# Performance work log

Hardware: AMD Instinct MI355X
Metric: run time of the kernel (lower is better)

The kernel has to match this reference:

```python
import jax, jax.numpy as jnp
import numpy as np
import math

TEMPERATURE = 1.0
TOP_K = 8
STALENESS_LAMBDA = 0.005
STALENESS_FLOOR = 0.1

B, F, H, E = 2048, 512, 256, 64


def setup_inputs() -> dict:
    key = jax.random.key(0)
    ks = jax.random.split(key, 9)
    return {
        "features": jax.random.normal(ks[0], (B, F), jnp.float32),
        "proj_w": jax.random.normal(ks[1], (H, F), jnp.float32) * (1.0 / math.sqrt(F)),
        "proj_b": jnp.zeros((H,), jnp.float32),
        "expert_emb": jax.random.normal(ks[2], (E, H), jnp.float32) * 0.1,  # nn.init.normal_(std=0.1)
        "expert_features": jax.random.normal(ks[3], (E, F), jnp.float32),
        "trust": jax.random.uniform(ks[4], (E,), jnp.float32, 0.1, 1.0),
        "staleness_dt": jax.random.uniform(ks[5], (E,), jnp.float32, 0.0, 600.0),  # seconds since update
        "fst_w": jax.random.normal(ks[6], (E, F, F), jnp.float32) * (1.0 / math.sqrt(F)),
        "fst_b": jnp.zeros((E, F), jnp.float32),
    }


def reference(features, proj_w, proj_b, expert_emb, expert_features, trust,
              staleness_dt, fst_w, fst_b):
    # --- learned gating: sigmoid(proj(x) . emb_j / sqrt(hidden_dim)) ---
    h = features @ proj_w.T + proj_b                      # [B,H]
    gate_logits = (h @ expert_emb.T) / jnp.sqrt(jnp.float32(h.shape[-1]))  # [B,E]
    gate = jax.nn.sigmoid(gate_logits)

    # --- similarity S_ij: cosine, clamped at 0 ---
    fn = features / jnp.maximum(jnp.linalg.norm(features, axis=1, keepdims=True), 1e-8)
    en = expert_features / jnp.maximum(jnp.linalg.norm(expert_features, axis=1, keepdims=True), 1e-8)
    sim = jnp.clip(fn @ en.T, 0.0, None)                  # [B,E]

    # --- staleness factor: max(floor, exp(-lambda * dt)) ---
    stale = jnp.maximum(STALENESS_FLOOR, jnp.exp(-STALENESS_LAMBDA * staleness_dt))  # [E]

    # --- final score: gate * T * S * staleness ---
    score = gate * sim * (trust * stale)[None, :]          # [B,E]

    # --- top-k expert selection + temperature softmax over selected ---
    top_v, top_i = jax.lax.top_k(score, TOP_K)             # [B,K]
    w = jax.nn.softmax(top_v / TEMPERATURE, axis=-1)       # [B,K]

    # --- per-expert FST (linear feature-space transform), MoE aggregation ---
    y = jnp.einsum('bf,efg->beg', features, fst_w) + fst_b[None]   # [B,E,F]
    yk = jnp.take_along_axis(y, top_i[:, :, None], axis=1)          # [B,K,F]
    out = jnp.einsum('bk,bkf->bf', w, yk)                           # [B,F]
    return out
```

## Files before the change

kernel.cpp:

```cpp
#include <hip/hip_runtime.h>
#include <hip/hip_fp16.h>
#include <math.h>

#define B_N 2048
#define F_N 512
#define H_N 256
#define E_N 64

typedef __attribute__((ext_vector_type(8))) _Float16 half8;
typedef __attribute__((ext_vector_type(4))) float f32x4;


__global__ __launch_bounds__(256) void k_prep(
    const float* __restrict__ proj_w, const float* __restrict__ expert_emb,
    const float* __restrict__ expert_features, const float* __restrict__ trust,
    const float* __restrict__ dt, const float* __restrict__ features,
    const float* __restrict__ fst_w, float* __restrict__ pwT,
    float* __restrict__ embT, float* __restrict__ enT,
    float* __restrict__ coef, int* __restrict__ cnt, _Float16* __restrict__ Fh,
    _Float16* __restrict__ Fl, float* __restrict__ fnorm,
    _Float16* __restrict__ WhT) {
  __shared__ float tile[16704];
  __shared__ float parts[4];
  int bid = blockIdx.x, tid = threadIdx.x;
  if (bid < 512) {
    int idx = bid * 256 + tid;
    int f = idx >> 8, h = idx & 255;
    pwT[idx] = proj_w[h * 512 + f];
    if (bid == 0 && tid < E_N) cnt[tid] = 0;
  } else if (bid < 576) {
    int e = bid - 512;
    float v0 = expert_features[e * 512 + tid];
    float v1 = expert_features[e * 512 + tid + 256];
    float ss = v0 * v0 + v1 * v1;
    #pragma unroll
    for (int off = 32; off; off >>= 1) ss += __shfl_xor(ss, off);
    if ((tid & 63) == 0) parts[tid >> 6] = ss;
    __syncthreads();
    float tot = parts[0] + parts[1] + parts[2] + parts[3];
    float inv = 1.0f / fmaxf(sqrtf(tot), 1e-8f);
    enT[tid * 64 + e] = v0 * inv;
    enT[(tid + 256) * 64 + e] = v1 * inv;
    embT[tid * 64 + e] = expert_emb[e * 256 + tid];
    if (tid == 0) {
      float st = fmaxf(0.1f, expf(-0.005f * dt[e]));
      coef[e] = trust[e] * st;
    }
  } else if (bid < 1088) {
    int gid = (bid - 576) * 256 + tid;
    int i = gid * 8;
    float4 v0 = *(const float4*)(features + i);
    float4 v1 = *(const float4*)(features + i + 4);
    float xs[8] = {v0.x, v0.y, v0.z, v0.w, v1.x, v1.y, v1.z, v1.w};
    half8 h, l;
    float ss = 0.0f;
    #pragma unroll
    for (int j = 0; j < 8; ++j) {
      h[j] = (_Float16)xs[j];
      l[j] = (_Float16)((xs[j] - (float)h[j]) * 2048.0f);
      ss = fmaf(xs[j], xs[j], ss);
    }
    *(half8*)(Fh + i) = h;
    *(half8*)(Fl + i) = l;
    #pragma unroll
    for (int off = 32; off; off >>= 1) ss += __shfl_xor(ss, off);
    if ((tid & 63) == 0) fnorm[gid >> 6] = ss;
  } else {
    int b2 = bid - 1088;
    int e = b2 >> 4;
    int kb = (b2 >> 1) & 7;
    int cb = b2 & 1;
    const float* src = fst_w + ((size_t)e << 18) + (size_t)(kb * 64) * 512 +
                       cb * 256;
    int kr = tid >> 6;
    int c4 = (tid & 63) * 4;
    #pragma unroll
    for (int r = 0; r < 16; ++r) {
      int k = r * 4 + kr;
      *(float4*)&tile[k * 260 + ((k >> 3) << 2) + c4] =
          *(const float4*)&src[(size_t)k * 512 + c4];
    }
    __syncthreads();
    int co = tid >> 3;
    int ko = (tid & 7) * 8;
    #pragma unroll
    for (int g = 0; g < 8; ++g) {
      int c = g * 32 + co;
      half8 vh;
      #pragma unroll
      for (int i = 0; i < 8; ++i) {
        int k = ko + i;
        vh[i] = (_Float16)tile[k * 260 + ((k >> 3) << 2) + c];
      }
      size_t dbase =
          ((size_t)e << 18) + (size_t)(cb * 256 + c) * 512 + kb * 64 + ko;
      *(half8*)(WhT + dbase) = vh;
    }
  }
}

__global__ __launch_bounds__(64) void k0gs(
    const float* __restrict__ pwT, const float* __restrict__ proj_b,
    const float* __restrict__ embT, const float* __restrict__ enT,
    _Float16* __restrict__ GhT, _Float16* __restrict__ GlT,
    float* __restrict__ gbias) {
  __shared__ float row[256];
  int f = blockIdx.x;
  int e = threadIdx.x;
  const float* src = (f < 512) ? (pwT + f * 256) : proj_b;
  *(float4*)&row[e * 4] = *(const float4*)&src[e * 4];
  __syncthreads();
  float g = 0.0f;
  #pragma unroll 8
  for (int h = 0; h < 256; ++h) g = fmaf(row[h], embT[h * 64 + e], g);
  if (f < 512) {
    _Float16 h0 = (_Float16)g;
    GhT[e * 512 + f] = h0;
    GlT[e * 512 + f] = (_Float16)((g - (float)h0) * 2048.0f);
    float en = enT[f * 64 + e];
    _Float16 h1 = (_Float16)en;
    GhT[(64 + e) * 512 + f] = h1;
    GlT[(64 + e) * 512 + f] = (_Float16)((en - (float)h1) * 2048.0f);
  } else {
    gbias[e] = g;
  }
}

__global__ __launch_bounds__(256) void k1_mfma(
    const _Float16* __restrict__ Fh, const _Float16* __restrict__ Fl,
    const _Float16* __restrict__ GhT, const _Float16* __restrict__ GlT,
    const float* __restrict__ fnorm, const float* __restrict__ coef,
    const float* __restrict__ gbias, int* __restrict__ cnt,
    int* __restrict__ tlist, float* __restrict__ wlist) {
  __shared__ _Float16 Bh[2][128 * 64];
  __shared__ _Float16 Bl[2][128 * 64];
  __shared__ _Float16 Ah[2][32 * 64];
  __shared__ _Float16 Al[2][32 * 64];

  int tid = threadIdx.x;
  int b0 = blockIdx.x * 32;
  int wave = tid >> 6, lane = tid & 63;

  size_t bsrc[4];
  int bdst[4];
  #pragma unroll
  for (int i = 0; i < 4; ++i) {
    int cw = wave * 32 + i * 8;
    int cl = cw + (lane >> 3);
    int g = (lane & 7) ^ (cl & 7);
    bsrc[i] = (size_t)cl * 512 + g * 8;
    bdst[i] = cw * 64;
  }
  int tw = wave * 8;
  int tkl = tw + (lane >> 3);
  int ga = (lane & 7) ^ (tkl & 7);
  size_t asrc = (size_t)(b0 + tkl) * 512 + ga * 8;
  int adst = tw * 64;

  f32x4 accH[2][2], accM[2][2];
  #pragma unroll
  for (int mt = 0; mt < 2; ++mt)
    #pragma unroll
    for (int ct = 0; ct < 2; ++ct) {
      accH[mt][ct] = (f32x4){0.f, 0.f, 0.f, 0.f};
      accM[mt][ct] = (f32x4){0.f, 0.f, 0.f, 0.f};
    }
  int kg = lane >> 4;
  int mrow = lane & 15;

  #define STG(K0S, BUF)                                                       \
    do {                                                                      \
      _Pragma("unroll")                                                       \
      for (int i = 0; i < 4; ++i) {                                           \
        __builtin_amdgcn_global_load_lds(                                     \
            (const __attribute__((address_space(1))) void*)(GhT + bsrc[i] + (K0S)), \
            (__attribute__((address_space(3))) void*)(&Bh[BUF][0] + bdst[i]), 16, 0, 0);\
        __builtin_amdgcn_global_load_lds(                                     \
            (const __attribute__((address_space(1))) void*)(GlT + bsrc[i] + (K0S)), \
            (__attribute__((address_space(3))) void*)(&Bl[BUF][0] + bdst[i]), 16, 0, 0);\
      }                                                                       \
      __builtin_amdgcn_global_load_lds(                                       \
          (const __attribute__((address_space(1))) void*)(Fh + asrc + (K0S)),  \
          (__attribute__((address_space(3))) void*)(&Ah[BUF][0] + adst), 16, 0, 0);\
      __builtin_amdgcn_global_load_lds(                                       \
          (const __attribute__((address_space(1))) void*)(Fl + asrc + (K0S)),  \
          (__attribute__((address_space(3))) void*)(&Al[BUF][0] + adst), 16, 0, 0);\
    } while (0)

  STG(0, 0);
  __syncthreads();
  int buf = 0;
  for (int s = 0; s < 8; ++s) {
    if (s < 7) STG((s + 1) * 64, buf ^ 1);
    #pragma unroll
    for (int kh = 0; kh < 2; ++kh) {
      int gq = kh * 4 + kg;
      half8 afh[2], afl[2], bfh[2], bfl[2];
      #pragma unroll
      for (int mt = 0; mt < 2; ++mt) {
        int tr = mt * 16 + mrow;
        int off = tr * 64 + ((gq ^ (tr & 7)) * 8);
        afh[mt] = *(const half8*)(&Ah[buf][0] + off);
        afl[mt] = *(const half8*)(&Al[buf][0] + off);
      }
      #pragma unroll
      for (int ct = 0; ct < 2; ++ct) {
        int cl = wave * 32 + ct * 16 + mrow;
        int off = cl * 64 + ((gq ^ (cl & 7)) * 8);
        bfh[ct] = *(const half8*)(&Bh[buf][0] + off);
        bfl[ct] = *(const half8*)(&Bl[buf][0] + off);
      }
      #pragma unroll
      for (int mt = 0; mt < 2; ++mt)
        #pragma unroll
        for (int ct = 0; ct < 2; ++ct) {
          accH[mt][ct] = __builtin_amdgcn_mfma_f32_16x16x32_f16(
              afh[mt], bfh[ct], accH[mt][ct], 0, 0, 0);
          accM[mt][ct] = __builtin_amdgcn_mfma_f32_16x16x32_f16(
              afh[mt], bfl[ct], accM[mt][ct], 0, 0, 0);
          accM[mt][ct] = __builtin_amdgcn_mfma_f32_16x16x32_f16(
              afl[mt], bfh[ct], accM[mt][ct], 0, 0, 0);
        }
    }
    __syncthreads();
    buf ^= 1;
  }
  #undef STG

  float* sc = (float*)&Bh[0][0];
  int rbase = (lane >> 4) * 4;
  #pragma unroll
  for (int mt = 0; mt < 2; ++mt)
    #pragma unroll
    for (int ct = 0; ct < 2; ++ct)
      #pragma unroll
      for (int r = 0; r < 4; ++r) {
        int tok = mt * 16 + rbase + r;
        int col = wave * 32 + ct * 16 + mrow;
        sc[tok * 128 + col] = accH[mt][ct][r] + accM[mt][ct][r] * (1.0f / 2048.0f);
      }
  __syncthreads();

  float cf = coef[lane];
  float gb = gbias[lane];
  for (int j = 0; j < 8; ++j) {
    int t = wave * 8 + j;
    int b = b0 + t;
    float l = sc[t * 128 + lane];
    float s = sc[t * 128 + 64 + lane];
    float inv_n = 1.0f / fmaxf(sqrtf(fnorm[b]), 1e-8f);
    float gate = 1.0f / (1.0f + expf(-(l + gb) * 0.0625f));
    float sim = fmaxf(s * inv_n, 0.0f);
    float score = gate * sim * cf;

    float cur = score;
    float bv[8];
    int bi[8];
    #pragma unroll
    for (int r = 0; r < 8; ++r) {
      float mv = cur;
      int mi = lane;
      #pragma unroll
      for (int off = 1; off < 64; off <<= 1) {
        float ov = __shfl_xor(mv, off);
        int oi = __shfl_xor(mi, off);
        if (ov > mv || (ov == mv && oi < mi)) { mv = ov; mi = oi; }
      }
      bv[r] = mv;
      bi[r] = mi;
      if (lane == mi) cur = -1.0f;
    }
    float m0 = bv[0];
    float ex[8];
    float sum = 0.0f;
    #pragma unroll
    for (int r = 0; r < 8; ++r) { ex[r] = expf(bv[r] - m0); sum += ex[r]; }
    float isum = 1.0f / sum;

    if (lane < 8) {
      int ir = 0; float er = 0.0f;
      switch (lane) {
        case 0: ir = bi[0]; er = ex[0]; break;
        case 1: ir = bi[1]; er = ex[1]; break;
        case 2: ir = bi[2]; er = ex[2]; break;
        case 3: ir = bi[3]; er = ex[3]; break;
        case 4: ir = bi[4]; er = ex[4]; break;
        case 5: ir = bi[5]; er = ex[5]; break;
        case 6: ir = bi[6]; er = ex[6]; break;
        case 7: ir = bi[7]; er = ex[7]; break;
      }
      float wr = er * isum;
      int pos = atomicAdd(&cnt[ir], 1);
      tlist[ir * B_N + pos] = b | (lane << 12);
      wlist[ir * B_N + pos] = wr;
    }
  }
}

__global__ __launch_bounds__(64) void k_sched(const int* __restrict__ cnt,
                                              int* __restrict__ jobs,
                                              int* __restrict__ njobs) {
  int e = threadIdx.x;
  int nt = (cnt[e] + 63) >> 6;
  int inc = nt;
  #pragma unroll
  for (int d = 1; d < 64; d <<= 1) {
    int v = __shfl_up(inc, d);
    if (e >= d) inc += v;
  }
  int base = inc - nt;
  for (int t = 0; t < nt; ++t) jobs[base + t] = (e << 8) | t;
  if (e == 63) njobs[0] = inc;
}

__global__ __launch_bounds__(256, 3) void k3_mfma(
    const _Float16* __restrict__ Fh, const _Float16* __restrict__ WhT,
    const float* __restrict__ fst_b, const int* __restrict__ cnt,
    const int* __restrict__ tlist, const float* __restrict__ wlist,
    const int* __restrict__ jobs, const int* __restrict__ njobs,
    float* __restrict__ ypart) {
  __shared__ _Float16 Bh[2][128 * 64];
  __shared__ _Float16 Ah[2][64 * 64];
  __shared__ int tl[64];
  __shared__ float wl[64];

  int tid = threadIdx.x;
  int job = blockIdx.x >> 2;
  int chunk = blockIdx.x & 3;
  if (job >= njobs[0]) return;
  int jb = jobs[job];
  int e = jb >> 8;
  int tile = jb & 255;
  int c0 = chunk * 128;
  int c_e = cnt[e];
  int t0 = tile * 64;

  if (tid < 64) {
    int t = t0 + tid;
    tl[tid] = tlist[e * B_N + (t < c_e ? t : t0)];
    wl[tid] = (t < c_e) ? wlist[e * B_N + t] : 0.0f;
  }
  __syncthreads();

  int wave = tid >> 6, lane = tid & 63;
  const _Float16* WhT_e = WhT + ((size_t)e << 18);

  size_t bsrc[4];
  int bdst[4];
  #pragma unroll
  for (int i = 0; i < 4; ++i) {
    int cw = wave * 32 + i * 8;
    int cl = cw + (lane >> 3);
    int g = (lane & 7) ^ (cl & 7);
    bsrc[i] = (size_t)(c0 + cl) * 512 + g * 8;
    bdst[i] = cw * 64;
  }
  size_t asrc[2];
  int adst[2];
  #pragma unroll
  for (int j = 0; j < 2; ++j) {
    int tw = wave * 16 + j * 8;
    int tkl = tw + (lane >> 3);
    int g = (lane & 7) ^ (tkl & 7);
    asrc[j] = (size_t)(tl[tkl] & 4095) * 512 + g * 8;
    adst[j] = tw * 64;
  }

  f32x4 acc[4][2];
  #pragma unroll
  for (int mt = 0; mt < 4; ++mt)
    #pragma unroll
    for (int ct = 0; ct < 2; ++ct) acc[mt][ct] = (f32x4){0.f, 0.f, 0.f, 0.f};

  int kg = lane >> 4;
  int mrow = lane & 15;

  #define STAGE(K0S, BUF)                                                     \
    do {                                                                      \
      _Pragma("unroll")                                                       \
      for (int i = 0; i < 4; ++i) {                                           \
        __builtin_amdgcn_global_load_lds(                                     \
            (const __attribute__((address_space(1))) void*)(WhT_e + bsrc[i] + (K0S)), \
            (__attribute__((address_space(3))) void*)(&Bh[BUF][0] + bdst[i]), 16, 0, 0);\
      }                                                                       \
      _Pragma("unroll")                                                       \
      for (int j = 0; j < 2; ++j) {                                           \
        __builtin_amdgcn_global_load_lds(                                     \
            (const __attribute__((address_space(1))) void*)(Fh + asrc[j] + (K0S)), \
            (__attribute__((address_space(3))) void*)(&Ah[BUF][0] + adst[j]), 16, 0, 0);\
      }                                                                       \
    } while (0)

  STAGE(0, 0);
  __syncthreads();

  int buf = 0;
  for (int s = 0; s < 8; ++s) {
    if (s < 7) STAGE((s + 1) * 64, buf ^ 1);
    #pragma unroll
    for (int kh = 0; kh < 2; ++kh) {
      int gq = kh * 4 + kg;
      half8 af[4], bf[2];
      #pragma unroll
      for (int mt = 0; mt < 4; ++mt) {
        int tr = mt * 16 + mrow;
        af[mt] = *(const half8*)(&Ah[buf][0] + tr * 64 + ((gq ^ (tr & 7)) * 8));
      }
      #pragma unroll
      for (int ct = 0; ct < 2; ++ct) {
        int cl = wave * 32 + ct * 16 + mrow;
        bf[ct] = *(const half8*)(&Bh[buf][0] + cl * 64 + ((gq ^ (cl & 7)) * 8));
      }
      #pragma unroll
      for (int mt = 0; mt < 4; ++mt)
        #pragma unroll
        for (int ct = 0; ct < 2; ++ct)
          acc[mt][ct] = __builtin_amdgcn_mfma_f32_16x16x32_f16(
              af[mt], bf[ct], acc[mt][ct], 0, 0, 0);
    }
    __syncthreads();
    buf ^= 1;
  }
  #undef STAGE

  int rbase = (lane >> 4) * 4;
  int colbase = c0 + wave * 32 + mrow;
  float bia0 = fst_b[e * 512 + colbase];
  float bia1 = fst_b[e * 512 + colbase + 16];
  #pragma unroll
  for (int mt = 0; mt < 4; ++mt) {
    #pragma unroll
    for (int r = 0; r < 4; ++r) {
      int tloc = mt * 16 + rbase + r;
      float w = wl[tloc];
      if (w != 0.0f) {
        int v = tl[tloc];
        int tok = v & 4095;
        int slot = v >> 12;
        float* yp = ypart + (((size_t)tok * 8 + slot) << 9) + colbase;
        yp[0] = w * (acc[mt][0][r] + bia0);
        yp[16] = w * (acc[mt][1][r] + bia1);
      }
    }
  }
}

__global__ __launch_bounds__(256) void k4_reduce(const float* __restrict__ ypart,
                                                 float* __restrict__ out) {
  int b = blockIdx.x, tid = threadIdx.x;
  #pragma unroll
  for (int q = 0; q < 2; ++q) {
    int f = tid + q * 256;
    float a = 0.0f;
    #pragma unroll
    for (int s = 0; s < 8; ++s) a += ypart[(((size_t)b * 8 + s) << 9) + f];
    out[(size_t)b * 512 + f] = a;
  }
}

__global__ __launch_bounds__(64) void k0g(
    const float* __restrict__ pwT, const float* __restrict__ proj_b,
    const float* __restrict__ embT, const float* __restrict__ enT,
    float* __restrict__ Gpack, float* __restrict__ gbias) {
  __shared__ float row[256];
  int f = blockIdx.x;
  int e = threadIdx.x;
  const float* src = (f < 512) ? (pwT + f * 256) : proj_b;
  *(float4*)&row[e * 4] = *(const float4*)&src[e * 4];
  __syncthreads();
  float g = 0.0f;
  #pragma unroll 8
  for (int h = 0; h < 256; ++h) g = fmaf(row[h], embT[h * 64 + e], g);
  if (f < 512) {
    Gpack[(f * 64 + e) * 2 + 0] = g;
    Gpack[(f * 64 + e) * 2 + 1] = enT[f * 64 + e];
  } else {
    gbias[e] = g;
  }
}

__global__ __launch_bounds__(256) void k1_score(
    const float* __restrict__ features, const float* __restrict__ Gpack,
    const float* __restrict__ gbias, const float* __restrict__ coef,
    int* __restrict__ cnt, int* __restrict__ tk_idx, float* __restrict__ tk_w,
    int* __restrict__ tlist, float* __restrict__ wlist) {
  __shared__ float Ft[2][512];
  __shared__ float pl[4][64];
  __shared__ float ps[4][64];
  __shared__ float pn[4];
  int tid = threadIdx.x;
  int b0 = blockIdx.x * 2;
  {
    int t = tid >> 7;
    int fo = (tid & 127) * 4;
    *(float4*)&Ft[t][fo] =
        *(const float4*)&features[(size_t)(b0 + t) * 512 + fo];
  }
  __syncthreads();
  int wave = tid >> 6, e = tid & 63;
  int tok = wave & 1;
  int f0 = (wave >> 1) * 256;
  float la = 0.f, lb = 0.f, sa = 0.f, sb = 0.f;
  #pragma unroll 4
  for (int f = f0; f < f0 + 256; f += 2) {
    float2 g0 = *(const float2*)&Gpack[(f * 64 + e) * 2];
    float2 g1 = *(const float2*)&Gpack[((f + 1) * 64 + e) * 2];
    float x0 = Ft[tok][f];
    float x1 = Ft[tok][f + 1];
    la = fmaf(x0, g0.x, la);
    sa = fmaf(x0, g0.y, sa);
    lb = fmaf(x1, g1.x, lb);
    sb = fmaf(x1, g1.y, sb);
  }
  float nn = 0.f;
  #pragma unroll
  for (int j = 0; j < 4; ++j) {
    float v = Ft[tok][f0 + e + 64 * j];
    nn = fmaf(v, v, nn);
  }
  #pragma unroll
  for (int off = 32; off; off >>= 1) nn += __shfl_xor(nn, off);
  pl[wave][e] = la + lb;
  ps[wave][e] = sa + sb;
  if (e == 0) pn[wave] = nn;
  __syncthreads();
  if (wave < 2) {
    int b = b0 + wave;
    float l = pl[wave][e] + pl[wave + 2][e];
    float s = ps[wave][e] + ps[wave + 2][e];
    float ntot = pn[wave] + pn[wave + 2];
    float inv_n = 1.0f / fmaxf(sqrtf(ntot), 1e-8f);
    float gate = 1.0f / (1.0f + expf(-(l + gbias[e]) * 0.0625f));
    float sim = fmaxf(s * inv_n, 0.0f);
    float score = gate * sim * coef[e];
    float cur = score;
    float bv[8];
    int bi[8];
    #pragma unroll
    for (int r = 0; r < 8; ++r) {
      float mv = cur;
      int mi = e;
      #pragma unroll
      for (int off = 1; off < 64; off <<= 1) {
        float ov = __shfl_xor(mv, off);
        int oi = __shfl_xor(mi, off);
        if (ov > mv || (ov == mv && oi < mi)) { mv = ov; mi = oi; }
      }
      bv[r] = mv;
      bi[r] = mi;
      if (e == mi) cur = -1.0f;
    }
    float m0 = bv[0];
    float ex[8];
    float sum = 0.0f;
    #pragma unroll
    for (int r = 0; r < 8; ++r) { ex[r] = expf(bv[r] - m0); sum += ex[r]; }
    float isum = 1.0f / sum;
    if (e < 8) {
      int ir = 0; float er = 0.0f;
      switch (e) {
        case 0: ir = bi[0]; er = ex[0]; break;
        case 1: ir = bi[1]; er = ex[1]; break;
        case 2: ir = bi[2]; er = ex[2]; break;
        case 3: ir = bi[3]; er = ex[3]; break;
        case 4: ir = bi[4]; er = ex[4]; break;
        case 5: ir = bi[5]; er = ex[5]; break;
        case 6: ir = bi[6]; er = ex[6]; break;
        case 7: ir = bi[7]; er = ex[7]; break;
      }
      float wr = er * isum;
      int pos = atomicAdd(&cnt[ir], 1);
      tlist[ir * B_N + pos] = b;
      wlist[ir * B_N + pos] = wr;
      tk_idx[b * 8 + e] = ir;
      tk_w[b * 8 + e] = wr;
    }
  }
}

__global__ __launch_bounds__(256) void k2_bias(
    const int* __restrict__ tk_idx, const float* __restrict__ tk_w,
    const float* __restrict__ fst_b, float* __restrict__ out) {
  int b = blockIdx.x, tid = threadIdx.x;
  int ir[8];
  float wr[8];
  #pragma unroll
  for (int r = 0; r < 8; ++r) {
    ir[r] = tk_idx[b * 8 + r];
    wr[r] = tk_w[b * 8 + r];
  }
  #pragma unroll
  for (int q = 0; q < 2; ++q) {
    int f = tid + q * 256;
    float a = 0.0f;
    #pragma unroll
    for (int r = 0; r < 8; ++r) a = fmaf(wr[r], fst_b[ir[r] * 512 + f], a);
    out[(size_t)b * 512 + f] = a;
  }
}

#define TM 64
#define TN 256
#define KC 16
__global__ __launch_bounds__(256, 2) void k3_fst(
    const float* __restrict__ features, const float* __restrict__ fst_w,
    const int* __restrict__ cnt, const int* __restrict__ tlist,
    const float* __restrict__ wlist, float* __restrict__ out) {
  __shared__ float Ws[2][KC][TN];
  __shared__ float Ft[2][KC][TM];
  __shared__ int tl[TM];
  __shared__ float wl[TM];

  int tid = threadIdx.x;
  int e = blockIdx.x & 63;
  int rest = blockIdx.x >> 6;
  int tile = rest >> 1;
  int ch = rest & 1;
  int c0 = ch * TN;
  int c_e = cnt[e];
  int t0 = tile * TM;
  if (t0 >= c_e) return;

  if (tid < TM) {
    int t = t0 + tid;
    if (t < c_e) {
      tl[tid] = tlist[e * B_N + t] & 4095;
      wl[tid] = wlist[e * B_N + t];
    } else {
      tl[tid] = tlist[e * B_N + t0] & 4095;
      wl[tid] = 0.0f;
    }
  }
  __syncthreads();

  const float* fw_e = fst_w + (size_t)e * (512 * 512);
  int wave = tid >> 6, lane = tid & 63;
  int tg = wave * 2 + (lane >> 5);
  int cg = lane & 31;
  int ft_t = tid >> 2;
  int ft_fq = tid & 3;
  const float* ft_src_row = features + (size_t)tl[ft_t] * 512;

  auto stageWs = [&](int kc, int buf) {
    int f0 = kc * KC;
    #pragma unroll
    for (int r = 0; r < 4; ++r) {
      int f = wave * 4 + r;
      const float* src = fw_e + (size_t)(f0 + f) * 512 + c0 + lane * 4;
      __builtin_amdgcn_global_load_lds(
          (const __attribute__((address_space(1))) void*)src,
          (__attribute__((address_space(3))) void*)&Ws[buf][f][0], 16, 0, 0);
    }
  };
  auto loadFt = [&](int kc) -> float4 {
    return *(const float4*)&ft_src_row[kc * KC + ft_fq * 4];
  };
  auto writeFt = [&](float4 v, int buf) {
    Ft[buf][ft_fq * 4 + 0][ft_t] = v.x;
    Ft[buf][ft_fq * 4 + 1][ft_t] = v.y;
    Ft[buf][ft_fq * 4 + 2][ft_t] = v.z;
    Ft[buf][ft_fq * 4 + 3][ft_t] = v.w;
  };

  float acc[8][8];
  #pragma unroll
  for (int j = 0; j < 8; ++j)
    #pragma unroll
    for (int i = 0; i < 8; ++i) acc[j][i] = 0.0f;

  auto compute = [&](int buf) {
    #pragma unroll 4
    for (int f = 0; f < KC; ++f) {
      float4 a0 = *(const float4*)&Ft[buf][f][tg * 8];
      float4 a1 = *(const float4*)&Ft[buf][f][tg * 8 + 4];
      float4 w0 = *(const float4*)&Ws[buf][f][cg * 4];
      float4 w1 = *(const float4*)&Ws[buf][f][cg * 4 + 128];
      float av[8] = {a0.x, a0.y, a0.z, a0.w, a1.x, a1.y, a1.z, a1.w};
      float wv[8] = {w0.x, w0.y, w0.z, w0.w, w1.x, w1.y, w1.z, w1.w};
      #pragma unroll
      for (int j = 0; j < 8; ++j)
        #pragma unroll
        for (int i = 0; i < 8; ++i)
          acc[j][i] = fmaf(av[j], wv[i], acc[j][i]);
    }
  };

  stageWs(0, 0);
  float4 rf = loadFt(0);
  writeFt(rf, 0);
  __syncthreads();

  for (int kc = 0; kc < 32; ++kc) {
    int cb = kc & 1, nb = cb ^ 1;
    float4 rn = make_float4(0.f, 0.f, 0.f, 0.f);
    if (kc < 31) {
      stageWs(kc + 1, nb);
      rn = loadFt(kc + 1);
    }
    compute(cb);
    if (kc < 31) writeFt(rn, nb);
    __syncthreads();
  }

  #pragma unroll
  for (int j = 0; j < 8; ++j) {
    int lt = tg * 8 + j;
    float w = wl[lt];
    if (w != 0.0f) {
      size_t orow = (size_t)tl[lt] * 512 + c0 + cg * 4;
      #pragma unroll
      for (int i = 0; i < 4; ++i) atomicAdd(&out[orow + i], w * acc[j][i]);
      #pragma unroll
      for (int i = 0; i < 4; ++i)
        atomicAdd(&out[orow + 128 + i], w * acc[j][i + 4]);
    }
  }
}

extern "C" void kernel_launch(void* const* d_in, const int* in_sizes, int n_in,
                              void* d_out, int out_size, void* d_ws,
                              size_t ws_size, hipStream_t stream) {
  const float* features = (const float*)d_in[0];
  const float* proj_w = (const float*)d_in[1];
  const float* proj_b = (const float*)d_in[2];
  const float* expert_emb = (const float*)d_in[3];
  const float* expert_features = (const float*)d_in[4];
  const float* trust = (const float*)d_in[5];
  const float* dt = (const float*)d_in[6];
  const float* fst_w = (const float*)d_in[7];
  const float* fst_b = (const float*)d_in[8];
  float* out = (float*)d_out;
  float* ws = (float*)d_ws;

  float* coef = ws;
  int* cnt = (int*)(ws + 64);
  float* gbias = ws + 128;
  int* njobs = (int*)(ws + 192);
  int* jobs = (int*)(ws + 256);
  int* tlist = (int*)(ws + 2304);
  float* wlist = ws + 133376;
  _Float16* Fh = (_Float16*)(ws + 264448);
  _Float16* WhT = (_Float16*)(ws + 788736);
  float* U = ws + 9177344;
  float* pwT = U;
  float* embT = U + 131072;
  float* enT = U + 147456;
  _Float16* Fl = (_Float16*)(U + 180224);
  _Float16* GhT = (_Float16*)(U + 704512);
  _Float16* GlT = (_Float16*)(U + 737280);
  float* fnorm = U + 770048;
  float* ypart = U;
  size_t need3 = (size_t)(9177344 + 8388608) * 4;

  if (ws_size >= need3) {
    hipLaunchKernelGGL(k_prep, dim3(2112), dim3(256), 0, stream, proj_w,
                       expert_emb, expert_features, trust, dt, features, fst_w,
                       pwT, embT, enT, coef, cnt, Fh, Fl, fnorm, WhT);
    hipLaunchKernelGGL(k0gs, dim3(513), dim3(64), 0, stream, pwT, proj_b,
                       embT, enT, GhT, GlT, gbias);
    hipLaunchKernelGGL(k1_mfma, dim3(64), dim3(256), 0, stream, Fh, Fl, GhT,
                       GlT, fnorm, coef, gbias, cnt, tlist, wlist);
    hipLaunchKernelGGL(k_sched, dim3(1), dim3(64), 0, stream, cnt, jobs,
                       njobs);
    hipLaunchKernelGGL(k3_mfma, dim3(2048), dim3(256), 0, stream, Fh, WhT,
                       fst_b, cnt, tlist, wlist, jobs, njobs, ypart);
    hipLaunchKernelGGL(k4_reduce, dim3(2048), dim3(256), 0, stream, ypart,
                       out);
  } else {
    float* pwT2 = ws;
    float* embT2 = pwT2 + 131072;
    float* enT2 = embT2 + 16384;
    float* coef2 = enT2 + 32768;
    int* cnt2 = (int*)(coef2 + 64);
    int* tk_idx = cnt2 + 64;
    float* tk_w = (float*)(tk_idx + 16384);
    int* tlist2 = (int*)(tk_w + 16384);
    float* wlist2 = (float*)(tlist2 + 131072);
    float* Gpack = wlist2 + 131072;
    float* gbias2 = Gpack + 65536;
    hipLaunchKernelGGL(k_prep, dim3(576), dim3(256), 0, stream, proj_w,
                       expert_emb, expert_features, trust, dt, features, fst_w,
                       pwT2, embT2, enT2, coef2, cnt2, (_Float16*)Gpack,
                       (_Float16*)Gpack, Gpack, (_Float16*)Gpack);
    hipLaunchKernelGGL(k0g, dim3(513), dim3(64), 0, stream, pwT2, proj_b,
                       embT2, enT2, Gpack, gbias2);
    hipLaunchKernelGGL(k1_score, dim3(1024), dim3(256), 0, stream, features,
                       Gpack, gbias2, coef2, cnt2, tk_idx, tk_w, tlist2,
                       wlist2);
    hipLaunchKernelGGL(k2_bias, dim3(2048), dim3(256), 0, stream, tk_idx,
                       tk_w, fst_b, out);
    hipLaunchKernelGGL(k3_fst, dim3(4096), dim3(256), 0, stream, features,
                       fst_w, cnt2, tlist2, wlist2, out);
  }
}
```

Before: 124.7 us.

## Split score GEMM over K chunks, rank-based top-k, per-expert gather scheduling

The scoring GEMM kernel now runs on 256 blocks instead of 64 by splitting the K dimension into four chunks, each writing partial scores to global memory. A separate kernel sums the partials, computes gate/sim scores, and picks the top-8 with a rank-counting pass instead of eight shuffle-reduction rounds. A per-expert gather kernel replaces the global-atomic token lists and the single-block scheduler, building jobs with one atomic per expert. This raises parallelism on a small, latency-bound stage, at the cost of an extra launch and a global round trip for the partial scores.

```diff
diff --git a/kernel.cpp b/kernel.cpp
--- a/kernel.cpp
+++ b/kernel.cpp
@@ -19,7 +19,7 @@
     float* __restrict__ embT, float* __restrict__ enT,
     float* __restrict__ coef, int* __restrict__ cnt, _Float16* __restrict__ Fh,
     _Float16* __restrict__ Fl, float* __restrict__ fnorm,
-    _Float16* __restrict__ WhT) {
+    _Float16* __restrict__ WhT, int* __restrict__ njobs) {
   __shared__ float tile[16704];
   __shared__ float parts[4];
   int bid = blockIdx.x, tid = threadIdx.x;
@@ -28,6 +28,7 @@
     int f = idx >> 8, h = idx & 255;
     pwT[idx] = proj_w[h * 512 + f];
     if (bid == 0 && tid < E_N) cnt[tid] = 0;
+    if (bid == 0 && tid == 64) njobs[0] = 0;
   } else if (bid < 576) {
     int e = bid - 512;
     float v0 = expert_features[e * 512 + tid];
@@ -126,19 +127,20 @@
   }
 }
 
-__global__ __launch_bounds__(256) void k1_mfma(
+__global__ __launch_bounds__(256, 2) void k1a_mfma(
     const _Float16* __restrict__ Fh, const _Float16* __restrict__ Fl,
     const _Float16* __restrict__ GhT, const _Float16* __restrict__ GlT,
-    const float* __restrict__ fnorm, const float* __restrict__ coef,
-    const float* __restrict__ gbias, int* __restrict__ cnt,
-    int* __restrict__ tlist, float* __restrict__ wlist) {
+    float* __restrict__ scores4) {
   __shared__ _Float16 Bh[2][128 * 64];
   __shared__ _Float16 Bl[2][128 * 64];
   __shared__ _Float16 Ah[2][32 * 64];
   __shared__ _Float16 Al[2][32 * 64];
 
   int tid = threadIdx.x;
-  int b0 = blockIdx.x * 32;
+  int kc = blockIdx.x & 3;
+  int tt = blockIdx.x >> 2;
+  int b0 = tt * 32;
+  int k0 = kc * 128;
   int wave = tid >> 6, lane = tid & 63;
 
   size_t bsrc[4];
@@ -148,13 +150,13 @@
     int cw = wave * 32 + i * 8;
     int cl = cw + (lane >> 3);
     int g = (lane & 7) ^ (cl & 7);
-    bsrc[i] = (size_t)cl * 512 + g * 8;
+    bsrc[i] = (size_t)cl * 512 + k0 + g * 8;
     bdst[i] = cw * 64;
   }
   int tw = wave * 8;
   int tkl = tw + (lane >> 3);
   int ga = (lane & 7) ^ (tkl & 7);
-  size_t asrc = (size_t)(b0 + tkl) * 512 + ga * 8;
+  size_t asrc = (size_t)(b0 + tkl) * 512 + k0 + ga * 8;
   int adst = tw * 64;
 
   f32x4 accH[2][2], accM[2][2];
@@ -190,8 +192,9 @@
   STG(0, 0);
   __syncthreads();
   int buf = 0;
-  for (int s = 0; s < 8; ++s) {
-    if (s < 7) STG((s + 1) * 64, buf ^ 1);
+  #pragma unroll
+  for (int s = 0; s < 2; ++s) {
+    if (s < 1) STG(64, 1);
     #pragma unroll
     for (int kh = 0; kh < 2; ++kh) {
       int gq = kh * 4 + kg;
@@ -227,7 +230,6 @@
   }
   #undef STG
 
-  float* sc = (float*)&Bh[0][0];
   int rbase = (lane >> 4) * 4;
   #pragma unroll
   for (int mt = 0; mt < 2; ++mt)
@@ -235,82 +237,80 @@
     for (int ct = 0; ct < 2; ++ct)
       #pragma unroll
       for (int r = 0; r < 4; ++r) {
-        int tok = mt * 16 + rbase + r;
+        int tok = b0 + mt * 16 + rbase + r;
         int col = wave * 32 + ct * 16 + mrow;
-        sc[tok * 128 + col] = accH[mt][ct][r] + accM[mt][ct][r] * (1.0f / 2048.0f);
+        scores4[((size_t)(kc * 2048 + tok) << 7) + col] =
+            accH[mt][ct][r] + accM[mt][ct][r] * (1.0f / 2048.0f);
       }
-  __syncthreads();
-
-  float cf = coef[lane];
-  float gb = gbias[lane];
-  for (int j = 0; j < 8; ++j) {
-    int t = wave * 8 + j;
-    int b = b0 + t;
-    float l = sc[t * 128 + lane];
-    float s = sc[t * 128 + 64 + lane];
-    float inv_n = 1.0f / fmaxf(sqrtf(fnorm[b]), 1e-8f);
-    float gate = 1.0f / (1.0f + expf(-(l + gb) * 0.0625f));
-    float sim = fmaxf(s * inv_n, 0.0f);
-    float score = gate * sim * cf;
-
-    float cur = score;
-    float bv[8];
-    int bi[8];
-    #pragma unroll
-    for (int r = 0; r < 8; ++r) {
-      float mv = cur;
-      int mi = lane;
-      #pragma unroll
-      for (int off = 1; off < 64; off <<= 1) {
-        float ov = __shfl_xor(mv, off);
-        int oi = __shfl_xor(mi, off);
-        if (ov > mv || (ov == mv && oi < mi)) { mv = ov; mi = oi; }
-      }
-      bv[r] = mv;
-      bi[r] = mi;
-      if (lane == mi) cur = -1.0f;
-    }
-    float m0 = bv[0];
-    float ex[8];
-    float sum = 0.0f;
-    #pragma unroll
-    for (int r = 0; r < 8; ++r) { ex[r] = expf(bv[r] - m0); sum += ex[r]; }
-    float isum = 1.0f / sum;
-
-    if (lane < 8) {
-      int ir = 0; float er = 0.0f;
-      switch (lane) {
-        case 0: ir = bi[0]; er = ex[0]; break;
-        case 1: ir = bi[1]; er = ex[1]; break;
-        case 2: ir = bi[2]; er = ex[2]; break;
-        case 3: ir = bi[3]; er = ex[3]; break;
-        case 4: ir = bi[4]; er = ex[4]; break;
-        case 5: ir = bi[5]; er = ex[5]; break;
-        case 6: ir = bi[6]; er = ex[6]; break;
-        case 7: ir = bi[7]; er = ex[7]; break;
-      }
-      float wr = er * isum;
-      int pos = atomicAdd(&cnt[ir], 1);
-      tlist[ir * B_N + pos] = b | (lane << 12);
-      wlist[ir * B_N + pos] = wr;
-    }
-  }
-}
-
-__global__ __launch_bounds__(64) void k_sched(const int* __restrict__ cnt,
-                                              int* __restrict__ jobs,
-                                              int* __restrict__ njobs) {
-  int e = threadIdx.x;
-  int nt = (cnt[e] + 63) >> 6;
-  int inc = nt;
-  #pragma unroll
-  for (int d = 1; d < 64; d <<= 1) {
-    int v = __shfl_up(inc, d);
-    if (e >= d) inc += v;
-  }
-  int base = inc - nt;
-  for (int t = 0; t < nt; ++t) jobs[base + t] = (e << 8) | t;
-  if (e == 63) njobs[0] = inc;
+}
+
+__global__ __launch_bounds__(256) void k1b_rank(
+    const float* __restrict__ scores4, const float* __restrict__ fnorm,
+    const float* __restrict__ coef, const float* __restrict__ gbias,
+    int* __restrict__ sel, float* __restrict__ selw) {
+  __shared__ float sc[4][64];
+  __shared__ float ex8[4][8];
+  int tid = threadIdx.x;
+  int wave = tid >> 6, lane = tid & 63;
+  int b = blockIdx.x * 4 + wave;
+
+  float l = 0.f, s = 0.f;
+  #pragma unroll
+  for (int kc = 0; kc < 4; ++kc) {
+    const float* row = scores4 + ((size_t)(kc * 2048 + b) << 7);
+    l += row[lane];
+    s += row[64 + lane];
+  }
+  float inv_n = 1.0f / fmaxf(sqrtf(fnorm[b]), 1e-8f);
+  float gate = 1.0f / (1.0f + expf(-(l + gbias[lane]) * 0.0625f));
+  float sim = fmaxf(s * inv_n, 0.0f);
+  float score = gate * sim * coef[lane];
+  sc[wave][lane] = score;
+
+  int rank = 0;
+  float mx = score;
+  #pragma unroll 8
+  for (int j = 0; j < 64; ++j) {
+    float sj = sc[wave][j];
+    rank += (sj > score || (sj == score && j < lane)) ? 1 : 0;
+    mx = fmaxf(mx, sj);
+  }
+  float ev = expf(score - mx);
+  if (rank < 8) ex8[wave][rank] = ev;
+  float sum = 0.f;
+  #pragma unroll
+  for (int r = 0; r < 8; ++r) sum += ex8[wave][r];
+  if (rank < 8) {
+    sel[b * 8 + rank] = lane;
+    selw[b * 8 + rank] = ev / sum;
+  }
+}
+
+__global__ __launch_bounds__(256) void k_gather(
+    const int* __restrict__ sel, const float* __restrict__ selw,
+    int* __restrict__ cnt, int* __restrict__ tlist, float* __restrict__ wlist,
+    int* __restrict__ jobs, int* __restrict__ njobs) {
+  __shared__ int lcnt;
+  int e = blockIdx.x;
+  int tid = threadIdx.x;
+  if (tid == 0) lcnt = 0;
+  __syncthreads();
+  for (int q = 0; q < 64; ++q) {
+    int i = q * 256 + tid;
+    if (sel[i] == e) {
+      int pos = atomicAdd(&lcnt, 1);
+      tlist[e * B_N + pos] = (i >> 3) | ((i & 7) << 12);
+      wlist[e * B_N + pos] = selw[i];
+    }
+  }
+  __syncthreads();
+  if (tid == 0) {
+    int c = lcnt;
+    cnt[e] = c;
+    int nt = (c + 63) >> 6;
+    int base = atomicAdd(njobs, nt);
+    for (int t = 0; t < nt; ++t) jobs[base + t] = (e << 8) | t;
+  }
 }
 
 __global__ __launch_bounds__(256, 3) void k3_mfma(
@@ -749,19 +749,24 @@
   _Float16* GhT = (_Float16*)(U + 704512);
   _Float16* GlT = (_Float16*)(U + 737280);
   float* fnorm = U + 770048;
+  float* scores4 = U + 772096;
+  int* sel = (int*)(U + 1820672);
+  float* selw = U + 1837056;
   float* ypart = U;
   size_t need3 = (size_t)(9177344 + 8388608) * 4;
 
   if (ws_size >= need3) {
     hipLaunchKernelGGL(k_prep, dim3(2112), dim3(256), 0, stream, proj_w,
                        expert_emb, expert_features, trust, dt, features, fst_w,
-                       pwT, embT, enT, coef, cnt, Fh, Fl, fnorm, WhT);
+                       pwT, embT, enT, coef, cnt, Fh, Fl, fnorm, WhT, njobs);
     hipLaunchKernelGGL(k0gs, dim3(513), dim3(64), 0, stream, pwT, proj_b,
                        embT, enT, GhT, GlT, gbias);
-    hipLaunchKernelGGL(k1_mfma, dim3(64), dim3(256), 0, stream, Fh, Fl, GhT,
-                       GlT, fnorm, coef, gbias, cnt, tlist, wlist);
-    hipLaunchKernelGGL(k_sched, dim3(1), dim3(64), 0, stream, cnt, jobs,
-                       njobs);
+    hipLaunchKernelGGL(k1a_mfma, dim3(256), dim3(256), 0, stream, Fh, Fl, GhT,
+                       GlT, scores4);
+    hipLaunchKernelGGL(k1b_rank, dim3(512), dim3(256), 0, stream, scores4,
+                       fnorm, coef, gbias, sel, selw);
+    hipLaunchKernelGGL(k_gather, dim3(64), dim3(256), 0, stream, sel, selw,
+                       cnt, tlist, wlist, jobs, njobs);
     hipLaunchKernelGGL(k3_mfma, dim3(2048), dim3(256), 0, stream, Fh, WhT,
                        fst_b, cnt, tlist, wlist, jobs, njobs, ypart);
     hipLaunchKernelGGL(k4_reduce, dim3(2048), dim3(256), 0, stream, ypart,
@@ -781,7 +786,8 @@
     hipLaunchKernelGGL(k_prep, dim3(576), dim3(256), 0, stream, proj_w,
                        expert_emb, expert_features, trust, dt, features, fst_w,
                        pwT2, embT2, enT2, coef2, cnt2, (_Float16*)Gpack,
-                       (_Float16*)Gpack, Gpack, (_Float16*)Gpack);
+                       (_Float16*)Gpack, Gpack, (_Float16*)Gpack,
+                       (int*)(gbias2 + 64));
     hipLaunchKernelGGL(k0g, dim3(513), dim3(64), 0, stream, pwT2, proj_b,
                        embT2, enT2, Gpack, gbias2);
     hipLaunchKernelGGL(k1_score, dim3(1024), dim3(256), 0, stream, features,
```

After: 101.5 us. 1.23x faster.
